# Kernel tuning notes

Hardware: AMD Instinct MI355X
Metric: run time of the kernel (lower is better)

## Reference

```python
import jax, jax.numpy as jnp
import numpy as np

B, N, F_IN, H, C = 64, 512, 128, 128, 10
RATIO, NEG_SLOPE, LAMB = 0.5, 0.2, 1.0
K1 = int(np.ceil(RATIO * N))    # 256 nodes kept after pool1
K2 = int(np.ceil(RATIO * K1))   # 128 nodes kept after pool2


def _gcn(x, adj, W, b):
    # PyG-style GCN: add remaining self loops (fill=1, existing self-loop
    # weights kept), symmetric normalization, aggregate, add bias.
    h = x @ W
    n = adj.shape[-1]
    eye = jnp.eye(n, dtype=adj.dtype)
    diag = jnp.diagonal(adj, axis1=1, axis2=2)
    diag = jnp.where(diag == 0, 1.0, diag)
    a = adj * (1.0 - eye) + diag[:, :, None] * eye
    deg = a.sum(-1)
    dinv = jnp.where(deg > 0, 1.0 / jnp.sqrt(deg), 0.0)
    a_n = dinv[:, :, None] * a * dinv[:, None, :]
    return a_n @ h + b


def _info_score(x, adj):
    # NodeInformationScore: self loops added with weight 0, so
    # out = x - D^{-1/2} A D^{-1/2} x ; score = sum |out| over features.
    deg = adj.sum(-1)
    dinv = jnp.where(deg > 0, 1.0 / jnp.sqrt(deg), 0.0)
    a_n = dinv[:, :, None] * adj * dinv[:, None, :]
    return jnp.abs(x - a_n @ x).sum(-1)


def _sparsemax(z, mask):
    # Row-wise sparsemax over masked entries (each row has >=1 valid entry
    # thanks to the self loop). Shift by row max (sparsemax is shift-invariant).
    n = z.shape[-1]
    big_neg = jnp.asarray(-1e30, z.dtype)
    zmax = jnp.max(jnp.where(mask, z, big_neg), axis=-1, keepdims=True)
    zc = z - zmax
    zs = jnp.where(mask, zc, big_neg)
    zsort = -jnp.sort(-zs, axis=-1)                    # descending
    kk = jnp.arange(1, n + 1, dtype=z.dtype)
    cum = jnp.cumsum(zsort, axis=-1)
    cond = (1.0 + kk * zsort) > cum
    rho = jnp.sum(cond, axis=-1, keepdims=True)        # support size >= 1
    cum_rho = jnp.take_along_axis(cum, rho - 1, axis=-1)
    tau = (cum_rho - 1.0) / rho.astype(z.dtype)
    return jnp.maximum(zc - tau, 0.0) * mask


def _pool(x, adj, att, k):
    # HGPSLPool (sample=True, sparse=True, sl=True, lamb=1.0).
    score = _info_score(x, adj)
    _, perm = jax.lax.top_k(score, k)                  # [B, k] top nodes per graph
    xp = jnp.take_along_axis(x, perm[:, :, None], axis=1)
    # k_hop=3 neighborhood augmentation (two TwoHopNeighborhood passes);
    # augmented-only edges get attr 0, original edges keep their weight.
    s = jax.lax.stop_gradient((adj > 0).astype(x.dtype))
    for _ in range(2):
        s = jnp.where(s + s @ s > 0, 1.0, 0.0)

    def sub(m):
        m = jnp.take_along_axis(m, perm[:, :, None], axis=1)
        return jnp.take_along_axis(m, perm[:, None, :], axis=2)

    sp = sub(s)
    ap = sub(adj)                                      # kept-edge attrs
    eye = jnp.eye(k, dtype=x.dtype)
    sp = jnp.maximum(sp, eye)                          # add remaining self loops (attr fill 0)
    mask = sp > 0
    hh = att.shape[0] // 2
    a_i = xp @ att[:hh]                                # [B, k]
    a_j = xp @ att[hh:]
    logits = jax.nn.leaky_relu(a_i[:, :, None] + a_j[:, None, :], NEG_SLOPE) + LAMB * ap
    new_adj = _sparsemax(logits, mask)                 # learned sparse row-stochastic adjacency
    return xp, new_adj


def _readout(h):
    # torch_geometric gmp / gap concatenated (all graphs have equal node count)
    return jnp.concatenate([h.max(axis=1), h.mean(axis=1)], axis=-1)


def _forward(x, adj, W1, b1, att1, W2, b2, att2, W3, b3, Wl1, bl1, Wl2, bl2, Wl3, bl3):
    h = jax.nn.relu(_gcn(x, adj, W1, b1))
    h, adj1 = _pool(h, adj, att1, K1)
    x1 = _readout(h)
    h = jax.nn.relu(_gcn(h, adj1, W2, b2))
    h, adj2 = _pool(h, adj1, att2, K2)
    x2 = _readout(h)
    h = jax.nn.relu(_gcn(h, adj2, W3, b3))
    x3 = _readout(h)
    z = jax.nn.relu(x1) + jax.nn.relu(x2) + jax.nn.relu(x3)
    z = jax.nn.relu(z @ Wl1 + bl1)
    z = jax.nn.relu(z @ Wl2 + bl2)
    return jax.nn.log_softmax(z @ Wl3 + bl3, axis=-1)


def setup_inputs() -> dict:
    key = jax.random.key(0)
    ks = jax.random.split(key, 10)
    r = jax.random.uniform(ks[0], (B, N, N))
    up = jnp.triu((r < 10.0 / N).astype(jnp.float32), k=1)
    adj = up + jnp.swapaxes(up, 1, 2)   # symmetric binary adj, no self loops, avg degree ~10
    x = jax.random.normal(ks[1], (B, N, F_IN), dtype=jnp.float32)

    def lin(k, fi, fo):
        return jax.random.normal(k, (fi, fo), dtype=jnp.float32) / np.sqrt(fi)

    return {
        "x": x, "adj": adj,
        "W1": lin(ks[2], F_IN, H), "b1": jnp.zeros((H,), jnp.float32),
        "att1": jax.random.normal(ks[3], (2 * H,), jnp.float32) * 0.1,
        "W2": lin(ks[4], H, H), "b2": jnp.zeros((H,), jnp.float32),
        "att2": jax.random.normal(ks[5], (2 * H,), jnp.float32) * 0.1,
        "W3": lin(ks[6], H, H), "b3": jnp.zeros((H,), jnp.float32),
        "Wl1": lin(ks[7], 2 * H, H), "bl1": jnp.zeros((H,), jnp.float32),
        "Wl2": lin(ks[8], H, H // 2), "bl2": jnp.zeros((H // 2,), jnp.float32),
        "Wl3": lin(ks[9], H // 2, C), "bl3": jnp.zeros((C,), jnp.float32),
    }


def reference(x, adj, W1, b1, att1, W2, b2, att2, W3, b3, Wl1, bl1, Wl2, bl2, Wl3, bl3):
    return _forward(x, adj, W1, b1, att1, W2, b2, att2, W3, b3,
                    Wl1, bl1, Wl2, bl2, Wl3, bl3)
```

## Files before the change

### kernel.cpp

```cpp
#include <hip/hip_runtime.h>
#include <math.h>

#define BB 64
#define N1 512
#define K1 256
#define K2 128
#define HF 128
#define NC 10

__device__ __forceinline__ int xcd_swizzle(int bid, int nwg) {
    return (bid & 7) * (nwg >> 3) + (bid >> 3);
}

__global__ __launch_bounds__(64) void deg_bits_kernel(const float* __restrict__ adj,
                                                      float* __restrict__ dinv_gcn,
                                                      float* __restrict__ dinv_info,
                                                      unsigned* __restrict__ bits,
                                                      float* __restrict__ adjval, int n) {
    int row = blockIdx.x;
    int i = row % n;
    const float* ar = adj + (size_t)row * n;
    float* av = adjval + (size_t)row * n;
    int lane = threadIdx.x;
    int W = n >> 5;
    unsigned* wrow = bits + (size_t)row * W;
    float s = 0.f;
    int base = 0;
    int kn = n >> 6;
    for (int k = 0; k < kn; k++) {
        float a = ar[k * 64 + lane];
        s += a;
        unsigned long long m = __ballot(a > 0.f);
        if (lane == 0) {
            wrow[2 * k]     = (unsigned)(m & 0xffffffffull);
            wrow[2 * k + 1] = (unsigned)(m >> 32);
        }
        if (a > 0.f) {
            int slot = base + (int)__popcll(m & ((1ull << lane) - 1ull));
            av[slot] = a;
        }
        base += (int)__popcll(m);
    }
    for (int off = 32; off > 0; off >>= 1) s += __shfl_down(s, off);
    if (lane == 0) {
        float diag = ar[i];
        float dg = s + (diag == 0.f ? 1.f : 0.f);
        dinv_info[row] = s  > 0.f ? 1.f / sqrtf(s)  : 0.f;
        dinv_gcn[row]  = dg > 0.f ? 1.f / sqrtf(dg) : 0.f;
    }
}

__global__ __launch_bounds__(256) void build_coef(const unsigned* __restrict__ bits,
                                                  float* __restrict__ adjval,
                                                  float* __restrict__ coefg,
                                                  const float* __restrict__ dinvg,
                                                  const float* __restrict__ dinvi,
                                                  int n) {
    int lane = threadIdx.x & 63;
    int row = blockIdx.x * 4 + (threadIdx.x >> 6);
    int b = row / n, i = row % n;
    int W = n >> 5;
    float* av = adjval + (size_t)row * n;
    float* cg = coefg + (size_t)row * n;
    const float* dg = dinvg + b * n;
    const float* di = dinvi + b * n;
    unsigned worig = (lane < W) ? bits[(size_t)row * W + lane] : 0u;
    unsigned w = worig;
    if ((i >> 5) == lane) w |= (1u << (i & 31));
    int pca = __popc(w), pco = __popc(worig);
    int sc = (pca << 16) | pco;
#pragma unroll
    for (int off = 1; off < 64; off <<= 1) {
        int t = __shfl_up(sc, off);
        if (lane >= off) sc += t;
    }
    int o  = (sc >> 16) - pca;
    int cb = (sc & 0xffff) - pco;
    unsigned mm = w;
    while (mm) {
        int bp = __ffs(mm) - 1;
        mm &= mm - 1;
        int j = (lane << 5) + bp;
        float a;
        if ((worig >> bp) & 1u) { a = av[cb]; av[cb] = a * di[j]; cb++; }
        else                    { a = 1.f; }
        cg[o] = a * dg[j];
        o++;
    }
}

__global__ __launch_bounds__(128) void gemm128(const float* __restrict__ X,
                                               const float* __restrict__ W,
                                               float* __restrict__ Y, int M) {
    __shared__ float xl[16 * 128];
    int f = threadIdx.x;
    int r0 = blockIdx.x * 16;
    for (int idx = f; idx < 16 * 128; idx += 128) {
        int r = idx >> 7, k = idx & 127;
        xl[idx] = X[(size_t)(r0 + r) * 128 + k];
    }
    __syncthreads();
    float acc[16];
#pragma unroll
    for (int r = 0; r < 16; r++) acc[r] = 0.f;
    for (int k = 0; k < 128; k++) {
        float w = W[k * 128 + f];
#pragma unroll
        for (int r = 0; r < 16; r++) acc[r] += xl[r * 128 + k] * w;
    }
#pragma unroll
    for (int r = 0; r < 16; r++) Y[(size_t)(r0 + r) * 128 + f] = acc[r];
}

__global__ __launch_bounds__(128) void gcn_agg(const float* __restrict__ coefg,
                                               const unsigned* __restrict__ bits,
                                               const float* __restrict__ dinvg,
                                               const float* __restrict__ hin,
                                               const float* __restrict__ bias,
                                               float* __restrict__ hout, int n) {
    __shared__ int idxl[512];
    __shared__ float coef[512];
    __shared__ int s_nnz;
    int row = xcd_swizzle(blockIdx.x, gridDim.x);
    int b = row / n, i = row % n;
    int tid = threadIdx.x;
    int W = n >> 5;
    const float* cgrow = coefg + (size_t)row * n;
    if (tid < 64) {
        int lane = tid;
        unsigned w = 0;
        if (lane < W) {
            w = bits[(size_t)row * W + lane];
            if ((i >> 5) == lane) w |= (1u << (i & 31));
        }
        int pc = __popc(w);
        int sc = pc;
#pragma unroll
        for (int off = 1; off < 64; off <<= 1) {
            int t = __shfl_up(sc, off);
            if (lane >= off) sc += t;
        }
        if (lane == 63) s_nnz = sc;
        int o = sc - pc;
        unsigned mm = w;
        while (mm) {
            int bp = __ffs(mm) - 1;
            mm &= mm - 1;
            int j = (lane << 5) + bp;
            idxl[o] = j;
            coef[o] = cgrow[o];
            o++;
        }
    }
    __syncthreads();
    int nnz = s_nnz;
    int f = tid;
    const float* hb = hin + (size_t)b * n * HF;
    float acc = 0.f;
    int it = 0;
    for (; it + 4 <= nnz; it += 4) {
        int j0 = idxl[it], j1 = idxl[it + 1], j2 = idxl[it + 2], j3 = idxl[it + 3];
        float v0 = hb[(size_t)j0 * HF + f];
        float v1 = hb[(size_t)j1 * HF + f];
        float v2 = hb[(size_t)j2 * HF + f];
        float v3 = hb[(size_t)j3 * HF + f];
        float c0 = coef[it], c1 = coef[it + 1], c2 = coef[it + 2], c3 = coef[it + 3];
        acc += c0 * v0; acc += c1 * v1; acc += c2 * v2; acc += c3 * v3;
    }
    for (; it < nnz; it++) {
        acc += coef[it] * hb[(size_t)idxl[it] * HF + f];
    }
    float di = dinvg[b * n + i];
    float v = di * acc + bias[f];
    hout[(size_t)row * HF + f] = fmaxf(v, 0.f);
}

__global__ __launch_bounds__(128) void info_score(const float* __restrict__ coefi,
                                                  const unsigned* __restrict__ bits,
                                                  const float* __restrict__ dinvi,
                                                  const float* __restrict__ h,
                                                  float* __restrict__ score, int n) {
    __shared__ int idxl[512];
    __shared__ float coef[512];
    __shared__ int s_nnz;
    __shared__ float red[128];
    int row = xcd_swizzle(blockIdx.x, gridDim.x);
    int b = row / n, i = row % n;
    int tid = threadIdx.x;
    int W = n >> 5;
    const float* cirow = coefi + (size_t)row * n;
    if (tid < 64) {
        int lane = tid;
        unsigned w = (lane < W) ? bits[(size_t)row * W + lane] : 0u;
        int pc = __popc(w);
        int sc = pc;
#pragma unroll
        for (int off = 1; off < 64; off <<= 1) {
            int t = __shfl_up(sc, off);
            if (lane >= off) sc += t;
        }
        if (lane == 63) s_nnz = sc;
        int o = sc - pc;
        unsigned mm = w;
        while (mm) {
            int bp = __ffs(mm) - 1;
            mm &= mm - 1;
            int j = (lane << 5) + bp;
            idxl[o] = j;
            coef[o] = cirow[o];
            o++;
        }
    }
    __syncthreads();
    int nnz = s_nnz;
    int f = tid;
    const float* hb = h + (size_t)b * n * HF;
    float acc = 0.f;
    int it = 0;
    for (; it + 4 <= nnz; it += 4) {
        int j0 = idxl[it], j1 = idxl[it + 1], j2 = idxl[it + 2], j3 = idxl[it + 3];
        float v0 = hb[(size_t)j0 * HF + f];
        float v1 = hb[(size_t)j1 * HF + f];
        float v2 = hb[(size_t)j2 * HF + f];
        float v3 = hb[(size_t)j3 * HF + f];
        float c0 = coef[it], c1 = coef[it + 1], c2 = coef[it + 2], c3 = coef[it + 3];
        acc += c0 * v0; acc += c1 * v1; acc += c2 * v2; acc += c3 * v3;
    }
    for (; it < nnz; it++) {
        acc += coef[it] * hb[(size_t)idxl[it] * HF + f];
    }
    float di = dinvi[b * n + i];
    float diff = fabsf(hb[(size_t)i * HF + f] - di * acc);
    red[f] = diff;
    __syncthreads();
    for (int s = 64; s > 0; s >>= 1) {
        if (f < s) red[f] += red[f + s];
        __syncthreads();
    }
    if (f == 0) score[row] = red[0];
}

template <int NN>
__global__ __launch_bounds__(NN) void topk_kernel(const float* __restrict__ score,
                                                  int* __restrict__ perm, int k) {
    __shared__ unsigned long long keys[NN];
    int b = blockIdx.x, t = threadIdx.x;
    unsigned u = __float_as_uint(score[b * NN + t]);
    unsigned asc = (u & 0x80000000u) ? ~u : (u | 0x80000000u);
    unsigned desc = ~asc;
    keys[t] = ((unsigned long long)desc << 32) | (unsigned)t;
    __syncthreads();
    for (int kk = 2; kk <= NN; kk <<= 1) {
        for (int j = kk >> 1; j > 0; j >>= 1) {
            int ixj = t ^ j;
            if (ixj > t) {
                bool up = ((t & kk) == 0);
                unsigned long long a = keys[t], c = keys[ixj];
                if ((a > c) == up) { keys[t] = c; keys[ixj] = a; }
            }
            __syncthreads();
        }
    }
    if (t < k) perm[b * k + t] = (int)(keys[t] & 0xffffffffu);
}

__global__ __launch_bounds__(128) void gather_rows(const float* __restrict__ h,
                                                   const int* __restrict__ perm,
                                                   float* __restrict__ xp, int n, int k) {
    int idx = blockIdx.x;
    int b = idx / k;
    int f = threadIdx.x;
    int pi = perm[idx];
    xp[(size_t)idx * HF + f] = h[((size_t)b * n + pi) * HF + f];
}

__global__ __launch_bounds__(64) void bits_expand(const unsigned* __restrict__ sin,
                                                  unsigned* __restrict__ sout, int n, int W) {
    __shared__ unsigned rowi[16];
    __shared__ int jlist[512];
    __shared__ unsigned res[64];
    __shared__ int s_nnz;
    int row = blockIdx.x;
    int b = row / n;
    int t = threadIdx.x;
    unsigned w = (t < W) ? sin[(size_t)row * W + t] : 0u;
    if (t < W) rowi[t] = w;
    int pc = __popc(w);
    int sc = pc;
#pragma unroll
    for (int off = 1; off < 64; off <<= 1) {
        int v = __shfl_up(sc, off);
        if (t >= off) sc += v;
    }
    if (t == 63) s_nnz = sc;
    int o = sc - pc;
    unsigned mm = w;
    while (mm) {
        int bp = __ffs(mm) - 1;
        mm &= mm - 1;
        jlist[o++] = (t << 5) + bp;
    }
    __syncthreads();
    int nnz = s_nnz;
    int JC = 64 / W;
    int chunk = t / W, wi = t % W;
    const unsigned* sb = sin + (size_t)b * n * W;
    unsigned r = 0;
    int q = chunk;
    for (; q + 3 * JC < nnz; q += 4 * JC) {
        int j0 = jlist[q], j1 = jlist[q + JC], j2 = jlist[q + 2 * JC], j3 = jlist[q + 3 * JC];
        unsigned v0 = sb[(size_t)j0 * W + wi];
        unsigned v1 = sb[(size_t)j1 * W + wi];
        unsigned v2 = sb[(size_t)j2 * W + wi];
        unsigned v3 = sb[(size_t)j3 * W + wi];
        r |= v0 | v1 | v2 | v3;
    }
    for (; q < nnz; q += JC) r |= sb[(size_t)jlist[q] * W + wi];
    res[t] = r;
    __syncthreads();
    if (t < W) {
        unsigned acc = rowi[t];
        for (int c = 0; c < JC; c++) acc |= res[c * W + t];
        sout[(size_t)row * W + t] = acc;
    }
}

__global__ __launch_bounds__(64) void bits_expand_perm(const unsigned* __restrict__ sin,
                                                       const int* __restrict__ perm,
                                                       unsigned* __restrict__ sout,
                                                       int n, int W, int k) {
    __shared__ unsigned rowi[16];
    __shared__ int jlist[512];
    __shared__ unsigned res[64];
    __shared__ int s_nnz;
    int r0 = blockIdx.x;
    int b = r0 / k;
    int pi = perm[r0];
    int t = threadIdx.x;
    size_t srow = (size_t)(b * n + pi) * W;
    unsigned w = (t < W) ? sin[srow + t] : 0u;
    if (t < W) rowi[t] = w;
    int pc = __popc(w);
    int sc = pc;
#pragma unroll
    for (int off = 1; off < 64; off <<= 1) {
        int v = __shfl_up(sc, off);
        if (t >= off) sc += v;
    }
    if (t == 63) s_nnz = sc;
    int o = sc - pc;
    unsigned mm = w;
    while (mm) {
        int bp = __ffs(mm) - 1;
        mm &= mm - 1;
        jlist[o++] = (t << 5) + bp;
    }
    __syncthreads();
    int nnz = s_nnz;
    int JC = 64 / W;
    int chunk = t / W, wi = t % W;
    const unsigned* sb = sin + (size_t)b * n * W;
    unsigned r = 0;
    int q = chunk;
    for (; q + 3 * JC < nnz; q += 4 * JC) {
        int j0 = jlist[q], j1 = jlist[q + JC], j2 = jlist[q + 2 * JC], j3 = jlist[q + 3 * JC];
        unsigned v0 = sb[(size_t)j0 * W + wi];
        unsigned v1 = sb[(size_t)j1 * W + wi];
        unsigned v2 = sb[(size_t)j2 * W + wi];
        unsigned v3 = sb[(size_t)j3 * W + wi];
        r |= v0 | v1 | v2 | v3;
    }
    for (; q < nnz; q += JC) r |= sb[(size_t)jlist[q] * W + wi];
    res[t] = r;
    __syncthreads();
    if (t < W) {
        unsigned acc = rowi[t];
        for (int c = 0; c < JC; c++) acc |= res[c * W + t];
        sout[(size_t)r0 * W + t] = acc;
    }
}

__global__ __launch_bounds__(128) void attn_dots(const float* __restrict__ xp,
                                                 const float* __restrict__ att,
                                                 float* __restrict__ ai, float* __restrict__ aj) {
    __shared__ float red[128];
    int idx = blockIdx.x;
    int f = threadIdx.x;
    float v = xp[(size_t)idx * HF + f];
    red[f] = v * att[f];
    __syncthreads();
    for (int s = 64; s > 0; s >>= 1) {
        if (f < s) red[f] += red[f + s];
        __syncthreads();
    }
    if (f == 0) ai[idx] = red[0];
    __syncthreads();
    red[f] = v * att[128 + f];
    __syncthreads();
    for (int s = 64; s > 0; s >>= 1) {
        if (f < s) red[f] += red[f + s];
        __syncthreads();
    }
    if (f == 0) aj[idx] = red[0];
}

template <int K>
__global__ __launch_bounds__(256) void sparsemax_wave(const float* __restrict__ ai,
                                                      const float* __restrict__ aj,
                                                      const int* __restrict__ perm,
                                                      const float* __restrict__ adjprev,
                                                      const unsigned* __restrict__ s4c,
                                                      float* __restrict__ newadj,
                                                      int nprev, int Wprev) {
    constexpr int EPL = K / 64;
    int lane = threadIdx.x & 63;
    int wid = threadIdx.x >> 6;
    int r = blockIdx.x * 4 + wid;
    int b = r / K, i = r % K;
    int pi = perm[r];
    float air = ai[r];
    const float* aprow = adjprev + ((size_t)b * nprev + pi) * nprev;
    const unsigned* srow = s4c + (size_t)r * Wprev;
    const int* permb = perm + b * K;
    const float* ajb = aj + b * K;

    float z[EPL], zc[EPL], zs[EPL];
    unsigned mbits = 0;
    float m = -1e30f;
#pragma unroll
    for (int e = 0; e < EPL; e++) {
        int j = lane * EPL + e;
        int pj = permb[j];
        float ap = aprow[pj];
        unsigned wb = srow[pj >> 5];
        bool mask = ((wb >> (pj & 31)) & 1u) || (i == j);
        float v = air + ajb[j];
        float lr = v > 0.f ? v : 0.2f * v;
        z[e] = lr + ap;
        if (mask) mbits |= (1u << e);
        m = fmaxf(m, mask ? z[e] : -1e30f);
    }
#pragma unroll
    for (int off = 1; off < 64; off <<= 1) m = fmaxf(m, __shfl_xor(m, off));

#pragma unroll
    for (int e = 0; e < EPL; e++) {
        zc[e] = z[e] - m;
        zs[e] = ((mbits >> e) & 1u) ? zc[e] : -1e30f;
    }

    for (int kk = 2; kk <= K; kk <<= 1) {
        for (int d = kk >> 1; d >= EPL; d >>= 1) {
            int lm = d / EPL;
#pragma unroll
            for (int e = 0; e < EPL; e++) {
                float other = __shfl_xor(zs[e], lm);
                int idx = lane * EPL + e;
                bool desc = (idx & kk) == 0;
                bool lower = (lane & lm) == 0;
                zs[e] = (desc == lower) ? fmaxf(zs[e], other) : fminf(zs[e], other);
            }
        }
#pragma unroll
        for (int dd = EPL >> 1; dd >= 1; dd >>= 1) {
            if (kk > dd) {
#pragma unroll
                for (int e = 0; e < EPL; e++) {
                    if (!(e & dd)) {
                        int ep = e | dd;
                        int idx = lane * EPL + e;
                        bool desc = (idx & kk) == 0;
                        float a = zs[e], c = zs[ep];
                        float mx = fmaxf(a, c), mn = fminf(a, c);
                        zs[e] = desc ? mx : mn;
                        zs[ep] = desc ? mn : mx;
                    }
                }
            }
        }
    }

    float c[EPL];
    c[0] = zs[0];
#pragma unroll
    for (int e = 1; e < EPL; e++) c[e] = c[e - 1] + zs[e];
    float lsum = c[EPL - 1];
    float sc = lsum;
#pragma unroll
    for (int off = 1; off < 64; off <<= 1) {
        float t = __shfl_up(sc, off);
        if (lane >= off) sc += t;
    }
    float excl = sc - lsum;
#pragma unroll
    for (int e = 0; e < EPL; e++) c[e] += excl;

    int cnt = 0;
#pragma unroll
    for (int e = 0; e < EPL; e++) {
        int idx = lane * EPL + e;
        if (1.f + (float)(idx + 1) * zs[e] > c[e]) cnt++;
    }
#pragma unroll
    for (int off = 1; off < 64; off <<= 1) cnt += __shfl_xor(cnt, off);
    int rho = cnt;

    int pos = rho - 1;
    int tl = pos / EPL, te = pos % EPL;
    float g[EPL];
#pragma unroll
    for (int e = 0; e < EPL; e++) g[e] = __shfl(c[e], tl);
    float cum_rho = g[0];
#pragma unroll
    for (int e = 1; e < EPL; e++) cum_rho = (te == e) ? g[e] : cum_rho;
    float tau = (cum_rho - 1.f) / (float)rho;

    float o[EPL];
#pragma unroll
    for (int e = 0; e < EPL; e++)
        o[e] = fmaxf(zc[e] - tau, 0.f) * (((mbits >> e) & 1u) ? 1.f : 0.f);

    float* orow = newadj + (size_t)r * K + lane * EPL;
    if constexpr (EPL == 4) {
        *reinterpret_cast<float4*>(orow) = make_float4(o[0], o[1], o[2], o[3]);
    } else {
        *reinterpret_cast<float2*>(orow) = make_float2(o[0], o[1]);
    }
}

__global__ __launch_bounds__(128) void readout_partial(const float* __restrict__ h,
                                                       float* __restrict__ pmax,
                                                       float* __restrict__ psum,
                                                       int n, int nch) {
    int blk = blockIdx.x;
    int c = blk % nch;
    int f = threadIdx.x;
    const float* hb = h + ((size_t)(blk / nch) * n + c * 32) * HF;
    float mx = -INFINITY, sm = 0.f;
#pragma unroll
    for (int i = 0; i < 32; i++) {
        float v = hb[(size_t)i * HF + f];
        mx = fmaxf(mx, v);
        sm += v;
    }
    pmax[(size_t)blk * HF + f] = mx;
    psum[(size_t)blk * HF + f] = sm;
}

__global__ __launch_bounds__(128) void readout_combine(const float* __restrict__ pmax,
                                                       const float* __restrict__ psum,
                                                       float* __restrict__ out,
                                                       int n, int nch) {
    int b = blockIdx.x;
    int f = threadIdx.x;
    float mx = -INFINITY, sm = 0.f;
    for (int c = 0; c < nch; c++) {
        mx = fmaxf(mx, pmax[((size_t)b * nch + c) * HF + f]);
        sm += psum[((size_t)b * nch + c) * HF + f];
    }
    out[b * 256 + f] = mx;
    out[b * 256 + 128 + f] = sm / (float)n;
}

__global__ __launch_bounds__(256) void mlp_kernel(const float* __restrict__ x1,
                                                  const float* __restrict__ x2,
                                                  const float* __restrict__ x3,
                                                  const float* __restrict__ Wl1,
                                                  const float* __restrict__ bl1,
                                                  const float* __restrict__ Wl2,
                                                  const float* __restrict__ bl2,
                                                  const float* __restrict__ Wl3,
                                                  const float* __restrict__ bl3,
                                                  float* __restrict__ out) {
    __shared__ float z[256];
    __shared__ float h1[128];
    __shared__ float h2[64];
    __shared__ float o[NC];
    int b = blockIdx.x;
    int t = threadIdx.x;
    z[t] = fmaxf(x1[b * 256 + t], 0.f) + fmaxf(x2[b * 256 + t], 0.f) + fmaxf(x3[b * 256 + t], 0.f);
    __syncthreads();
    if (t < 128) {
        float acc = bl1[t];
        for (int k = 0; k < 256; k++) acc += z[k] * Wl1[k * 128 + t];
        h1[t] = fmaxf(acc, 0.f);
    }
    __syncthreads();
    if (t < 64) {
        float acc = bl2[t];
        for (int k = 0; k < 128; k++) acc += h1[k] * Wl2[k * 64 + t];
        h2[t] = fmaxf(acc, 0.f);
    }
    __syncthreads();
    if (t < NC) {
        float acc = bl3[t];
        for (int k = 0; k < 64; k++) acc += h2[k] * Wl3[k * NC + t];
        o[t] = acc;
    }
    __syncthreads();
    if (t == 0) {
        float mx = o[0];
        for (int c = 1; c < NC; c++) mx = fmaxf(mx, o[c]);
        float s = 0.f;
        for (int c = 0; c < NC; c++) s += expf(o[c] - mx);
        float lse = mx + logf(s);
        for (int c = 0; c < NC; c++) out[b * NC + c] = o[c] - lse;
    }
}

extern "C" void kernel_launch(void* const* d_in, const int* in_sizes, int n_in,
                              void* d_out, int out_size, void* d_ws, size_t ws_size,
                              hipStream_t stream) {
    const float* x    = (const float*)d_in[0];
    const float* adj  = (const float*)d_in[1];
    const float* W1   = (const float*)d_in[2];
    const float* b1   = (const float*)d_in[3];
    const float* att1 = (const float*)d_in[4];
    const float* W2   = (const float*)d_in[5];
    const float* b2   = (const float*)d_in[6];
    const float* att2 = (const float*)d_in[7];
    const float* W3   = (const float*)d_in[8];
    const float* b3   = (const float*)d_in[9];
    const float* Wl1  = (const float*)d_in[10];
    const float* bl1  = (const float*)d_in[11];
    const float* Wl2  = (const float*)d_in[12];
    const float* bl2  = (const float*)d_in[13];
    const float* Wl3  = (const float*)d_in[14];
    const float* bl3  = (const float*)d_in[15];
    float* out = (float*)d_out;

    char* wp = (char*)d_ws;
    auto allocf = [&](size_t n) { float* r = (float*)wp; wp += n * sizeof(float); return r; };
    auto alloci = [&](size_t n) { int* r = (int*)wp; wp += n * sizeof(int); return r; };
    auto allocu = [&](size_t n) { unsigned* r = (unsigned*)wp; wp += n * sizeof(unsigned); return r; };

    float* dinvg1    = allocf(BB * N1);
    float* dinvi1    = allocf(BB * N1);
    float* hw        = allocf((size_t)BB * N1 * HF);
    float* h1        = allocf((size_t)BB * N1 * HF);
    float* score1    = allocf(BB * N1);
    int*   perm1     = alloci(BB * K1);
    float* xp1       = allocf((size_t)BB * K1 * HF);
    unsigned* bitsA  = allocu((size_t)BB * N1 * 16);
    unsigned* bitsB  = allocu((size_t)BB * N1 * 16);
    float* adjval    = allocf((size_t)BB * N1 * N1);
    float* coefg     = allocf((size_t)BB * N1 * N1);
    float* ai1       = allocf(BB * K1);
    float* aj1       = allocf(BB * K1);
    float* adj1      = allocf((size_t)BB * K1 * K1);
    float* x1r       = allocf(BB * 256);
    float* dinvg2    = allocf(BB * K1);
    float* dinvi2    = allocf(BB * K1);
    float* h2        = allocf((size_t)BB * K1 * HF);
    float* score2    = allocf(BB * K1);
    int*   perm2     = alloci(BB * K2);
    float* xp2       = allocf((size_t)BB * K2 * HF);
    float* ai2       = allocf(BB * K2);
    float* aj2       = allocf(BB * K2);
    float* adj2      = allocf((size_t)BB * K2 * K2);
    float* x2r       = allocf(BB * 256);
    float* dinvg3    = allocf(BB * K2);
    float* dinvi3    = allocf(BB * K2);
    float* h3        = allocf((size_t)BB * K2 * HF);
    float* x3r       = allocf(BB * 256);
    float* pmax      = allocf((size_t)BB * 8 * HF);
    float* psum      = allocf((size_t)BB * 8 * HF);

    deg_bits_kernel<<<dim3(BB * N1), dim3(64), 0, stream>>>(adj, dinvg1, dinvi1, bitsA, adjval, N1);
    build_coef<<<dim3(BB * N1 / 4), dim3(256), 0, stream>>>(bitsA, adjval, coefg, dinvg1, dinvi1, N1);
    gemm128<<<dim3(BB * N1 / 16), dim3(128), 0, stream>>>(x, W1, hw, BB * N1);
    gcn_agg<<<dim3(BB * N1), dim3(128), 0, stream>>>(coefg, bitsA, dinvg1, hw, b1, h1, N1);
    info_score<<<dim3(BB * N1), dim3(128), 0, stream>>>(adjval, bitsA, dinvi1, h1, score1, N1);
    topk_kernel<512><<<dim3(BB), dim3(512), 0, stream>>>(score1, perm1, K1);
    gather_rows<<<dim3(BB * K1), dim3(128), 0, stream>>>(h1, perm1, xp1, N1, K1);
    bits_expand<<<dim3(BB * N1), dim3(64), 0, stream>>>(bitsA, bitsB, N1, 16);
    bits_expand_perm<<<dim3(BB * K1), dim3(64), 0, stream>>>(bitsB, perm1, bitsA, N1, 16, K1);
    attn_dots<<<dim3(BB * K1), dim3(128), 0, stream>>>(xp1, att1, ai1, aj1);
    sparsemax_wave<K1><<<dim3(BB * K1 / 4), dim3(256), 0, stream>>>(ai1, aj1, perm1, adj, bitsA, adj1, N1, 16);
    readout_partial<<<dim3(BB * (K1 / 32)), dim3(128), 0, stream>>>(xp1, pmax, psum, K1, K1 / 32);
    readout_combine<<<dim3(BB), dim3(128), 0, stream>>>(pmax, psum, x1r, K1, K1 / 32);

    deg_bits_kernel<<<dim3(BB * K1), dim3(64), 0, stream>>>(adj1, dinvg2, dinvi2, bitsA, adjval, K1);
    build_coef<<<dim3(BB * K1 / 4), dim3(256), 0, stream>>>(bitsA, adjval, coefg, dinvg2, dinvi2, K1);
    gemm128<<<dim3(BB * K1 / 16), dim3(128), 0, stream>>>(xp1, W2, hw, BB * K1);
    gcn_agg<<<dim3(BB * K1), dim3(128), 0, stream>>>(coefg, bitsA, dinvg2, hw, b2, h2, K1);
    info_score<<<dim3(BB * K1), dim3(128), 0, stream>>>(adjval, bitsA, dinvi2, h2, score2, K1);
    topk_kernel<256><<<dim3(BB), dim3(256), 0, stream>>>(score2, perm2, K2);
    gather_rows<<<dim3(BB * K2), dim3(128), 0, stream>>>(h2, perm2, xp2, K1, K2);
    bits_expand<<<dim3(BB * K1), dim3(64), 0, stream>>>(bitsA, bitsB, K1, 8);
    bits_expand_perm<<<dim3(BB * K2), dim3(64), 0, stream>>>(bitsB, perm2, bitsA, K1, 8, K2);
    attn_dots<<<dim3(BB * K2), dim3(128), 0, stream>>>(xp2, att2, ai2, aj2);
    sparsemax_wave<K2><<<dim3(BB * K2 / 4), dim3(256), 0, stream>>>(ai2, aj2, perm2, adj1, bitsA, adj2, K1, 8);
    readout_partial<<<dim3(BB * (K2 / 32)), dim3(128), 0, stream>>>(xp2, pmax, psum, K2, K2 / 32);
    readout_combine<<<dim3(BB), dim3(128), 0, stream>>>(pmax, psum, x2r, K2, K2 / 32);

    deg_bits_kernel<<<dim3(BB * K2), dim3(64), 0, stream>>>(adj2, dinvg3, dinvi3, bitsB, adjval, K2);
    build_coef<<<dim3(BB * K2 / 4), dim3(256), 0, stream>>>(bitsB, adjval, coefg, dinvg3, dinvi3, K2);
    gemm128<<<dim3(BB * K2 / 16), dim3(128), 0, stream>>>(xp2, W3, hw, BB * K2);
    gcn_agg<<<dim3(BB * K2), dim3(128), 0, stream>>>(coefg, bitsB, dinvg3, hw, b3, h3, K2);
    readout_partial<<<dim3(BB * (K2 / 32)), dim3(128), 0, stream>>>(h3, pmax, psum, K2, K2 / 32);
    readout_combine<<<dim3(BB), dim3(128), 0, stream>>>(pmax, psum, x3r, K2, K2 / 32);

    mlp_kernel<<<dim3(BB), dim3(256), 0, stream>>>(x1r, x2r, x3r, Wl1, bl1, Wl2, bl2, Wl3, bl3, out);
}
```

Baseline: 521.3 us.

## Fuse coefficient build into gcn_agg/info_score and process one row per wave

Removes the build_coef kernel and its coefg buffer by computing the normalized coefficients inline inside gcn_agg and info_score, reading the raw compacted adjacency values. Both kernels now handle four rows per 256-thread block, one row per wave, with each lane doing two features via float2 loads. The info_score reduction switches from a shared-memory tree to wave shuffles. This cuts three launches and a dense N×N coefficient write and read, at the cost of duplicating the coefficient computation across the two kernels.

Result: faster. 470.6 us (-9.7%).

```diff
diff --git a/kernel.cpp b/kernel.cpp
--- a/kernel.cpp
+++ b/kernel.cpp
@@ -50,45 +50,6 @@
     }
 }
 
-__global__ __launch_bounds__(256) void build_coef(const unsigned* __restrict__ bits,
-                                                  float* __restrict__ adjval,
-                                                  float* __restrict__ coefg,
-                                                  const float* __restrict__ dinvg,
-                                                  const float* __restrict__ dinvi,
-                                                  int n) {
-    int lane = threadIdx.x & 63;
-    int row = blockIdx.x * 4 + (threadIdx.x >> 6);
-    int b = row / n, i = row % n;
-    int W = n >> 5;
-    float* av = adjval + (size_t)row * n;
-    float* cg = coefg + (size_t)row * n;
-    const float* dg = dinvg + b * n;
-    const float* di = dinvi + b * n;
-    unsigned worig = (lane < W) ? bits[(size_t)row * W + lane] : 0u;
-    unsigned w = worig;
-    if ((i >> 5) == lane) w |= (1u << (i & 31));
-    int pca = __popc(w), pco = __popc(worig);
-    int sc = (pca << 16) | pco;
-#pragma unroll
-    for (int off = 1; off < 64; off <<= 1) {
-        int t = __shfl_up(sc, off);
-        if (lane >= off) sc += t;
-    }
-    int o  = (sc >> 16) - pca;
-    int cb = (sc & 0xffff) - pco;
-    unsigned mm = w;
-    while (mm) {
-        int bp = __ffs(mm) - 1;
-        mm &= mm - 1;
-        int j = (lane << 5) + bp;
-        float a;
-        if ((worig >> bp) & 1u) { a = av[cb]; av[cb] = a * di[j]; cb++; }
-        else                    { a = 1.f; }
-        cg[o] = a * dg[j];
-        o++;
-    }
-}
-
 __global__ __launch_bounds__(128) void gemm128(const float* __restrict__ X,
                                                const float* __restrict__ W,
                                                float* __restrict__ Y, int M) {
@@ -112,132 +73,135 @@
     for (int r = 0; r < 16; r++) Y[(size_t)(r0 + r) * 128 + f] = acc[r];
 }
 
-__global__ __launch_bounds__(128) void gcn_agg(const float* __restrict__ coefg,
+__global__ __launch_bounds__(256) void gcn_agg(const float* __restrict__ adjval,
                                                const unsigned* __restrict__ bits,
                                                const float* __restrict__ dinvg,
                                                const float* __restrict__ hin,
                                                const float* __restrict__ bias,
                                                float* __restrict__ hout, int n) {
-    __shared__ int idxl[512];
-    __shared__ float coef[512];
-    __shared__ int s_nnz;
-    int row = xcd_swizzle(blockIdx.x, gridDim.x);
+    __shared__ int idxl[4][512];
+    __shared__ float coef[4][512];
+    int blk = xcd_swizzle(blockIdx.x, gridDim.x);
+    int wid = threadIdx.x >> 6;
+    int lane = threadIdx.x & 63;
+    int row = blk * 4 + wid;
     int b = row / n, i = row % n;
-    int tid = threadIdx.x;
     int W = n >> 5;
-    const float* cgrow = coefg + (size_t)row * n;
-    if (tid < 64) {
-        int lane = tid;
-        unsigned w = 0;
-        if (lane < W) {
-            w = bits[(size_t)row * W + lane];
-            if ((i >> 5) == lane) w |= (1u << (i & 31));
-        }
-        int pc = __popc(w);
-        int sc = pc;
-#pragma unroll
-        for (int off = 1; off < 64; off <<= 1) {
-            int t = __shfl_up(sc, off);
-            if (lane >= off) sc += t;
-        }
-        if (lane == 63) s_nnz = sc;
-        int o = sc - pc;
-        unsigned mm = w;
-        while (mm) {
-            int bp = __ffs(mm) - 1;
-            mm &= mm - 1;
-            int j = (lane << 5) + bp;
-            idxl[o] = j;
-            coef[o] = cgrow[o];
-            o++;
-        }
-    }
-    __syncthreads();
-    int nnz = s_nnz;
-    int f = tid;
-    const float* hb = hin + (size_t)b * n * HF;
-    float acc = 0.f;
+    const float* avrow = adjval + (size_t)row * n;
+    const float* dg = dinvg + b * n;
+    unsigned worig = (lane < W) ? bits[(size_t)row * W + lane] : 0u;
+    unsigned w = worig;
+    if ((i >> 5) == lane) w |= (1u << (i & 31));
+    int pca = __popc(w), pco = __popc(worig);
+    int sc = (pca << 16) | pco;
+#pragma unroll
+    for (int off = 1; off < 64; off <<= 1) {
+        int t = __shfl_up(sc, off);
+        if (lane >= off) sc += t;
+    }
+    int nnz = __shfl(sc, 63) >> 16;
+    int o  = (sc >> 16) - pca;
+    int cb = (sc & 0xffff) - pco;
+    unsigned mm = w;
+    while (mm) {
+        int bp = __ffs(mm) - 1;
+        mm &= mm - 1;
+        int j = (lane << 5) + bp;
+        float a = ((worig >> bp) & 1u) ? avrow[cb++] : 1.f;
+        idxl[wid][o] = j;
+        coef[wid][o] = a * dg[j];
+        o++;
+    }
+    __syncthreads();
+    const float* hf = hin + (size_t)b * n * HF + 2 * lane;
+    float ax = 0.f, ay = 0.f;
     int it = 0;
     for (; it + 4 <= nnz; it += 4) {
-        int j0 = idxl[it], j1 = idxl[it + 1], j2 = idxl[it + 2], j3 = idxl[it + 3];
-        float v0 = hb[(size_t)j0 * HF + f];
-        float v1 = hb[(size_t)j1 * HF + f];
-        float v2 = hb[(size_t)j2 * HF + f];
-        float v3 = hb[(size_t)j3 * HF + f];
-        float c0 = coef[it], c1 = coef[it + 1], c2 = coef[it + 2], c3 = coef[it + 3];
-        acc += c0 * v0; acc += c1 * v1; acc += c2 * v2; acc += c3 * v3;
+        int j0 = idxl[wid][it], j1 = idxl[wid][it + 1], j2 = idxl[wid][it + 2], j3 = idxl[wid][it + 3];
+        float2 v0 = *(const float2*)(hf + (size_t)j0 * HF);
+        float2 v1 = *(const float2*)(hf + (size_t)j1 * HF);
+        float2 v2 = *(const float2*)(hf + (size_t)j2 * HF);
+        float2 v3 = *(const float2*)(hf + (size_t)j3 * HF);
+        float c0 = coef[wid][it], c1 = coef[wid][it + 1], c2 = coef[wid][it + 2], c3 = coef[wid][it + 3];
+        ax += c0 * v0.x; ay += c0 * v0.y;
+        ax += c1 * v1.x; ay += c1 * v1.y;
+        ax += c2 * v2.x; ay += c2 * v2.y;
+        ax += c3 * v3.x; ay += c3 * v3.y;
     }
     for (; it < nnz; it++) {
-        acc += coef[it] * hb[(size_t)idxl[it] * HF + f];
-    }
-    float di = dinvg[b * n + i];
-    float v = di * acc + bias[f];
-    hout[(size_t)row * HF + f] = fmaxf(v, 0.f);
-}
-
-__global__ __launch_bounds__(128) void info_score(const float* __restrict__ coefi,
+        int j = idxl[wid][it];
+        float c = coef[wid][it];
+        float2 v = *(const float2*)(hf + (size_t)j * HF);
+        ax += c * v.x; ay += c * v.y;
+    }
+    float di = dg[i];
+    float bx = bias[2 * lane], by = bias[2 * lane + 1];
+    float2 outv = make_float2(fmaxf(di * ax + bx, 0.f), fmaxf(di * ay + by, 0.f));
+    *(float2*)(hout + (size_t)row * HF + 2 * lane) = outv;
+}
+
+__global__ __launch_bounds__(256) void info_score(const float* __restrict__ adjval,
                                                   const unsigned* __restrict__ bits,
                                                   const float* __restrict__ dinvi,
                                                   const float* __restrict__ h,
                                                   float* __restrict__ score, int n) {
-    __shared__ int idxl[512];
-    __shared__ float coef[512];
-    __shared__ int s_nnz;
-    __shared__ float red[128];
-    int row = xcd_swizzle(blockIdx.x, gridDim.x);
+    __shared__ int idxl[4][512];
+    __shared__ float coef[4][512];
+    int blk = xcd_swizzle(blockIdx.x, gridDim.x);
+    int wid = threadIdx.x >> 6;
+    int lane = threadIdx.x & 63;
+    int row = blk * 4 + wid;
     int b = row / n, i = row % n;
-    int tid = threadIdx.x;
     int W = n >> 5;
-    const float* cirow = coefi + (size_t)row * n;
-    if (tid < 64) {
-        int lane = tid;
-        unsigned w = (lane < W) ? bits[(size_t)row * W + lane] : 0u;
-        int pc = __popc(w);
-        int sc = pc;
-#pragma unroll
-        for (int off = 1; off < 64; off <<= 1) {
-            int t = __shfl_up(sc, off);
-            if (lane >= off) sc += t;
-        }
-        if (lane == 63) s_nnz = sc;
-        int o = sc - pc;
-        unsigned mm = w;
-        while (mm) {
-            int bp = __ffs(mm) - 1;
-            mm &= mm - 1;
-            int j = (lane << 5) + bp;
-            idxl[o] = j;
-            coef[o] = cirow[o];
-            o++;
-        }
-    }
-    __syncthreads();
-    int nnz = s_nnz;
-    int f = tid;
-    const float* hb = h + (size_t)b * n * HF;
-    float acc = 0.f;
+    const float* avrow = adjval + (size_t)row * n;
+    const float* di_ = dinvi + b * n;
+    unsigned w = (lane < W) ? bits[(size_t)row * W + lane] : 0u;
+    int pc = __popc(w);
+    int sc = pc;
+#pragma unroll
+    for (int off = 1; off < 64; off <<= 1) {
+        int t = __shfl_up(sc, off);
+        if (lane >= off) sc += t;
+    }
+    int nnz = __shfl(sc, 63);
+    int o = sc - pc;
+    unsigned mm = w;
+    while (mm) {
+        int bp = __ffs(mm) - 1;
+        mm &= mm - 1;
+        int j = (lane << 5) + bp;
+        idxl[wid][o] = j;
+        coef[wid][o] = avrow[o] * di_[j];
+        o++;
+    }
+    __syncthreads();
+    const float* hf = h + (size_t)b * n * HF + 2 * lane;
+    float ax = 0.f, ay = 0.f;
     int it = 0;
     for (; it + 4 <= nnz; it += 4) {
-        int j0 = idxl[it], j1 = idxl[it + 1], j2 = idxl[it + 2], j3 = idxl[it + 3];
-        float v0 = hb[(size_t)j0 * HF + f];
-        float v1 = hb[(size_t)j1 * HF + f];
-        float v2 = hb[(size_t)j2 * HF + f];
-        float v3 = hb[(size_t)j3 * HF + f];
-        float c0 = coef[it], c1 = coef[it + 1], c2 = coef[it + 2], c3 = coef[it + 3];
-        acc += c0 * v0; acc += c1 * v1; acc += c2 * v2; acc += c3 * v3;
+        int j0 = idxl[wid][it], j1 = idxl[wid][it + 1], j2 = idxl[wid][it + 2], j3 = idxl[wid][it + 3];
+        float2 v0 = *(const float2*)(hf + (size_t)j0 * HF);
+        float2 v1 = *(const float2*)(hf + (size_t)j1 * HF);
+        float2 v2 = *(const float2*)(hf + (size_t)j2 * HF);
+        float2 v3 = *(const float2*)(hf + (size_t)j3 * HF);
+        float c0 = coef[wid][it], c1 = coef[wid][it + 1], c2 = coef[wid][it + 2], c3 = coef[wid][it + 3];
+        ax += c0 * v0.x; ay += c0 * v0.y;
+        ax += c1 * v1.x; ay += c1 * v1.y;
+        ax += c2 * v2.x; ay += c2 * v2.y;
+        ax += c3 * v3.x; ay += c3 * v3.y;
     }
     for (; it < nnz; it++) {
-        acc += coef[it] * hb[(size_t)idxl[it] * HF + f];
-    }
-    float di = dinvi[b * n + i];
-    float diff = fabsf(hb[(size_t)i * HF + f] - di * acc);
-    red[f] = diff;
-    __syncthreads();
-    for (int s = 64; s > 0; s >>= 1) {
-        if (f < s) red[f] += red[f + s];
-        __syncthreads();
-    }
-    if (f == 0) score[row] = red[0];
+        int j = idxl[wid][it];
+        float c = coef[wid][it];
+        float2 v = *(const float2*)(hf + (size_t)j * HF);
+        ax += c * v.x; ay += c * v.y;
+    }
+    float dii = di_[i];
+    float2 hself = *(const float2*)(hf + (size_t)i * HF);
+    float r = fabsf(hself.x - dii * ax) + fabsf(hself.y - dii * ay);
+#pragma unroll
+    for (int off = 1; off < 64; off <<= 1) r += __shfl_xor(r, off);
+    if (lane == 0) score[row] = r;
 }
 
 template <int NN>
@@ -644,7 +608,6 @@
     unsigned* bitsA  = allocu((size_t)BB * N1 * 16);
     unsigned* bitsB  = allocu((size_t)BB * N1 * 16);
     float* adjval    = allocf((size_t)BB * N1 * N1);
-    float* coefg     = allocf((size_t)BB * N1 * N1);
     float* ai1       = allocf(BB * K1);
     float* aj1       = allocf(BB * K1);
     float* adj1      = allocf((size_t)BB * K1 * K1);
@@ -667,10 +630,9 @@
     float* psum      = allocf((size_t)BB * 8 * HF);
 
     deg_bits_kernel<<<dim3(BB * N1), dim3(64), 0, stream>>>(adj, dinvg1, dinvi1, bitsA, adjval, N1);
-    build_coef<<<dim3(BB * N1 / 4), dim3(256), 0, stream>>>(bitsA, adjval, coefg, dinvg1, dinvi1, N1);
     gemm128<<<dim3(BB * N1 / 16), dim3(128), 0, stream>>>(x, W1, hw, BB * N1);
-    gcn_agg<<<dim3(BB * N1), dim3(128), 0, stream>>>(coefg, bitsA, dinvg1, hw, b1, h1, N1);
-    info_score<<<dim3(BB * N1), dim3(128), 0, stream>>>(adjval, bitsA, dinvi1, h1, score1, N1);
+    gcn_agg<<<dim3(BB * N1 / 4), dim3(256), 0, stream>>>(adjval, bitsA, dinvg1, hw, b1, h1, N1);
+    info_score<<<dim3(BB * N1 / 4), dim3(256), 0, stream>>>(adjval, bitsA, dinvi1, h1, score1, N1);
     topk_kernel<512><<<dim3(BB), dim3(512), 0, stream>>>(score1, perm1, K1);
     gather_rows<<<dim3(BB * K1), dim3(128), 0, stream>>>(h1, perm1, xp1, N1, K1);
     bits_expand<<<dim3(BB * N1), dim3(64), 0, stream>>>(bitsA, bitsB, N1, 16);
@@ -681,10 +643,9 @@
     readout_combine<<<dim3(BB), dim3(128), 0, stream>>>(pmax, psum, x1r, K1, K1 / 32);
 
     deg_bits_kernel<<<dim3(BB * K1), dim3(64), 0, stream>>>(adj1, dinvg2, dinvi2, bitsA, adjval, K1);
-    build_coef<<<dim3(BB * K1 / 4), dim3(256), 0, stream>>>(bitsA, adjval, coefg, dinvg2, dinvi2, K1);
     gemm128<<<dim3(BB * K1 / 16), dim3(128), 0, stream>>>(xp1, W2, hw, BB * K1);
-    gcn_agg<<<dim3(BB * K1), dim3(128), 0, stream>>>(coefg, bitsA, dinvg2, hw, b2, h2, K1);
-    info_score<<<dim3(BB * K1), dim3(128), 0, stream>>>(adjval, bitsA, dinvi2, h2, score2, K1);
+    gcn_agg<<<dim3(BB * K1 / 4), dim3(256), 0, stream>>>(adjval, bitsA, dinvg2, hw, b2, h2, K1);
+    info_score<<<dim3(BB * K1 / 4), dim3(256), 0, stream>>>(adjval, bitsA, dinvi2, h2, score2, K1);
     topk_kernel<256><<<dim3(BB), dim3(256), 0, stream>>>(score2, perm2, K2);
     gather_rows<<<dim3(BB * K2), dim3(128), 0, stream>>>(h2, perm2, xp2, K1, K2);
     bits_expand<<<dim3(BB * K1), dim3(64), 0, stream>>>(bitsA, bitsB, K1, 8);
@@ -695,9 +656,8 @@
     readout_combine<<<dim3(BB), dim3(128), 0, stream>>>(pmax, psum, x2r, K2, K2 / 32);
 
     deg_bits_kernel<<<dim3(BB * K2), dim3(64), 0, stream>>>(adj2, dinvg3, dinvi3, bitsB, adjval, K2);
-    build_coef<<<dim3(BB * K2 / 4), dim3(256), 0, stream>>>(bitsB, adjval, coefg, dinvg3, dinvi3, K2);
     gemm128<<<dim3(BB * K2 / 16), dim3(128), 0, stream>>>(xp2, W3, hw, BB * K2);
-    gcn_agg<<<dim3(BB * K2), dim3(128), 0, stream>>>(coefg, bitsB, dinvg3, hw, b3, h3, K2);
+    gcn_agg<<<dim3(BB * K2 / 4), dim3(256), 0, stream>>>(adjval, bitsB, dinvg3, hw, b3, h3, K2);
     readout_partial<<<dim3(BB * (K2 / 32)), dim3(128), 0, stream>>>(h3, pmax, psum, K2, K2 / 32);
     readout_combine<<<dim3(BB), dim3(128), 0, stream>>>(pmax, psum, x3r, K2, K2 / 32);
 
```
